# Kernel tuning notes

Measured on AMD Instinct MI355X. Metric: run time of the kernel, lower is better.

## Reference

```python
import jax, jax.numpy as jnp
import numpy as np

B, S, NX, NH = 2, 2048, 1024, 16
HD = NX // NH  # head dim = 64


def setup_inputs() -> dict:
    key = jax.random.key(0)
    k1, k2, k3 = jax.random.split(key, 3)
    x = jax.random.normal(k1, (B, S, NX), dtype=jnp.float32)
    w_attn = jax.random.normal(k2, (NX, 3 * NX), dtype=jnp.float32) * 0.02
    b_attn = jnp.zeros((3 * NX,), dtype=jnp.float32)
    w_proj = jax.random.normal(k3, (NX, NX), dtype=jnp.float32) * 0.02
    b_proj = jnp.zeros((NX,), dtype=jnp.float32)
    return {"x": x, "w_attn": w_attn, "b_attn": b_attn, "w_proj": w_proj, "b_proj": b_proj}


def _split_heads(t):
    # [B, S, NX] -> [B, NH, S, HD]
    b, s, _ = t.shape
    return t.reshape(b, s, NH, HD).transpose(0, 2, 1, 3)


def reference(x, w_attn, b_attn, w_proj, b_proj):
    # c_attn: Conv1D == affine projection to fused QKV
    qkv = jnp.einsum("bsi,io->bso", x, w_attn) + b_attn  # [B, S, 3*NX]
    q, k, v = jnp.split(qkv, 3, axis=2)
    q, k, v = _split_heads(q), _split_heads(k), _split_heads(v)  # [B, NH, S, HD]

    # scaled dot-product scores (scale=True)
    w = jnp.einsum("bhqd,bhkd->bhqk", q, k) / jnp.sqrt(jnp.asarray(HD, dtype=q.dtype))

    # causal mask via multiply-subtract (matches TF: w*b - 10000*(1-b))
    nd = ns = S
    i = jnp.arange(nd)[:, None]
    j = jnp.arange(ns)[None, :]
    b = (i >= j - ns + nd).astype(w.dtype)  # [nd, ns]
    w = w * b - 10000.0 * (1.0 - b)

    w = jax.nn.softmax(w, axis=-1)  # stable_softmax
    # attn_dropout / head_mask: identity (inference, no head mask)

    a = jnp.einsum("bhqk,bhkd->bhqd", w, v)  # [B, NH, S, HD]
    # merge heads -> [B, S, NX]
    a = a.transpose(0, 2, 1, 3).reshape(B, S, NX)
    # c_proj
    out = jnp.einsum("bsi,io->bso", a, w_proj) + b_proj
    return out
```

## Files before the change

### kernel.cpp

```cpp
#include <hip/hip_runtime.h>
#include <stdint.h>

typedef __attribute__((ext_vector_type(8))) short short8;
typedef __attribute__((ext_vector_type(4))) float f32x4;
typedef __attribute__((ext_vector_type(16))) float f32x16;
typedef __attribute__((ext_vector_type(4))) unsigned short ushort4v;
typedef __attribute__((ext_vector_type(2))) int int2v;

#define BB 2
#define SS 2048
#define NXDIM 1024
#define NHEADS 16
#define HDIM 64

__device__ __forceinline__ unsigned short f2bf(float f){
  unsigned int u = __float_as_uint(f);
  u += 0x7fffu + ((u >> 16) & 1u);
  return (unsigned short)(u >> 16);
}

__device__ __forceinline__ void gload_lds16(const void* g, void* l){
  __builtin_amdgcn_global_load_lds((const __attribute__((address_space(1))) void*)g,
                                   (__attribute__((address_space(3))) void*)l, 16, 0, 0);
}

__device__ __forceinline__ unsigned cvt_pk_bf16(float lo, float hi){
  unsigned r;
  asm("v_cvt_pk_bf16_f32 %0, %1, %2" : "=v"(r) : "v"(lo), "v"(hi));
  return r;
}

__device__ __forceinline__ int2v ds_tr_b16(unsigned addr){
  int2v r;
  asm volatile("ds_read_b64_tr_b16 %0, %1" : "=v"(r) : "v"(addr));
  return r;
}

__device__ __forceinline__ int2v plswap(int a, int b){
  return __builtin_amdgcn_permlane32_swap(a, b, false, false);
}
__device__ __forceinline__ float plmax(float x){
  int2v r = plswap(__float_as_int(x), __float_as_int(x));
  return fmaxf(__int_as_float(r.x), __int_as_float(r.y));
}
__device__ __forceinline__ float pladd(float x){
  int2v r = plswap(__float_as_int(x), __float_as_int(x));
  return __int_as_float(r.x) + __int_as_float(r.y);
}

__global__ __launch_bounds__(256) void prep_k(const float* __restrict__ x,
                                              unsigned short* __restrict__ xb,
                                              const float* __restrict__ wa,
                                              unsigned short* __restrict__ waT,
                                              const float* __restrict__ wp,
                                              unsigned short* __restrict__ wpT){
  __shared__ float t[32][33];
  int bid = blockIdx.x;
  if (bid < 4096){
    const int i = bid*256 + (int)threadIdx.x;
    float4 v = ((const float4*)x)[i];
    ushort4v r = { f2bf(v.x), f2bf(v.y), f2bf(v.z), f2bf(v.w) };
    ((ushort4v*)xb)[i] = r;
    return;
  }
  bid -= 4096;
  const int by = (bid >> 7) * 32;
  int bxi = bid & 127;
  const bool second = bxi >= 96;
  const float* in = second ? wp : wa;
  unsigned short* out = second ? wpT : waT;
  const int C = second ? 1024 : 3072;
  const int R = 1024;
  const int bx = (second ? (bxi - 96) : bxi) * 32;
  const int tx = threadIdx.x & 31, ty = threadIdx.x >> 5;
  #pragma unroll
  for (int i = ty; i < 32; i += 8)
    t[i][tx] = in[(size_t)(by + i) * C + bx + tx];
  __syncthreads();
  #pragma unroll
  for (int i = ty; i < 32; i += 8)
    out[(size_t)(bx + i) * R + by + tx] = f2bf(t[tx][i]);
}

__global__ __launch_bounds__(256) void gemm2_64_k(const unsigned short* __restrict__ A,
                                                  const unsigned short* __restrict__ BT,
                                                  const float* __restrict__ bias,
                                                  float* __restrict__ Cout,
                                                  int M, int N, int K)
{
  __shared__ unsigned short As[64*32];
  __shared__ unsigned short Bs[64*32];
  const int tid = threadIdx.x;
  const int w = tid >> 6, lane = tid & 63;
  const int l15 = lane & 15, g = lane >> 4;
  const int wr = w >> 1, wc = w & 1;
  const int m0 = blockIdx.y * 64, n0 = blockIdx.x * 64;

  f32x4 acc[2][2];
  #pragma unroll
  for (int m=0;m<2;m++)
    #pragma unroll
    for (int n=0;n<2;n++) acc[m][n] = (f32x4){0.f,0.f,0.f,0.f};

  const int srow_in = lane >> 2;
  const int scol = (lane & 3) * 8;

  for (int k0 = 0; k0 < K; k0 += 32){
    __syncthreads();
    gload_lds16(A  + (size_t)(m0 + w*16 + srow_in) * K + (k0 + scol), &As[(w*16)*32]);
    gload_lds16(BT + (size_t)(n0 + w*16 + srow_in) * K + (k0 + scol), &Bs[(w*16)*32]);
    __syncthreads();

    short8 af[2], bf[2];
    #pragma unroll
    for (int m=0;m<2;m++) af[m] = *(const short8*)&As[(wr*32 + m*16 + l15)*32 + g*8];
    #pragma unroll
    for (int n=0;n<2;n++) bf[n] = *(const short8*)&Bs[(wc*32 + n*16 + l15)*32 + g*8];
    #pragma unroll
    for (int m=0;m<2;m++)
      #pragma unroll
      for (int n=0;n<2;n++)
        acc[m][n] = __builtin_amdgcn_mfma_f32_16x16x32_bf16(af[m], bf[n], acc[m][n], 0, 0, 0);
  }

  const int crow0 = m0 + wr*32;
  const int ccol0 = n0 + wc*32;
  #pragma unroll
  for (int n=0;n<2;n++){
    const int col = ccol0 + n*16 + l15;
    const float bv = bias[col];
    #pragma unroll
    for (int m=0;m<2;m++){
      #pragma unroll
      for (int r=0;r<4;r++){
        const int row = crow0 + m*16 + g*4 + r;
        Cout[(size_t)row * N + col] = acc[m][n][r] + bv;
      }
    }
  }
}

__global__ __launch_bounds__(512) void gemm256_k(const unsigned short* __restrict__ A,
                                                 const unsigned short* __restrict__ BT,
                                                 const float* __restrict__ bias,
                                                 unsigned short* __restrict__ Cout,
                                                 int M, int N, int K)
{
  __shared__ unsigned short lds[57344];
  unsigned short* As0 = lds;
  unsigned short* Bs0 = lds + 32768;
  const int tid = threadIdx.x;
  const int w = tid >> 6, lane = tid & 63;
  const int l15 = lane & 15, g = lane >> 4;
  const int wm = w >> 2, wn = w & 3;
  const int m0 = blockIdx.y * 256, n0 = blockIdx.x * 192;

  f32x4 acc[8][3];
  #pragma unroll
  for (int m=0;m<8;m++)
    #pragma unroll
    for (int n=0;n<3;n++) acc[m][n] = (f32x4){0.f,0.f,0.f,0.f};

  const int srow = lane >> 3;
  const int scol = 8 * ((lane & 7) ^ (lane >> 3));

  auto stageA = [&](int bi, int k0, int j){
    const int r = w*32 + j*8 + srow;
    gload_lds16(A + (size_t)(m0 + r) * K + (k0 + scol), As0 + bi*16384 + (w*32 + j*8)*64);
  };
  auto stageB = [&](int bi, int k0, int j){
    const int r = w*24 + j*8 + srow;
    gload_lds16(BT + (size_t)(n0 + r) * K + (k0 + scol), Bs0 + bi*12288 + (w*24 + j*8)*64);
  };

  #pragma unroll
  for (int j=0;j<4;j++) stageA(0, 0, j);
  #pragma unroll
  for (int j=0;j<3;j++) stageB(0, 0, j);
  asm volatile("s_waitcnt vmcnt(0)" ::: "memory");
  __syncthreads();

  const int niter = K >> 6;
  int cur = 0;

  for (int t = 0; t < niter; ++t){
    const int k1 = (t+1) << 6;
    if (t+1 < niter){
      #pragma unroll
      for (int j=0;j<4;j++) stageA(cur^1, k1, j);
      #pragma unroll
      for (int j=0;j<3;j++) stageB(cur^1, k1, j);
    }

    const char* Ab = (const char*)(As0 + cur*16384);
    const char* Bb = (const char*)(Bs0 + cur*12288);

    short8 bf[3][2];
    #pragma unroll
    for (int nf=0;nf<3;nf++){
      const int row = wn*48 + nf*16 + l15;
      #pragma unroll
      for (int kk=0;kk<2;kk++)
        bf[nf][kk] = *(const short8*)(Bb + row*128 + ((kk*64 + g*16) ^ ((l15&7)<<4)));
    }

    #pragma unroll
    for (int ph=0; ph<4; ++ph){
      short8 af[2][2];
      #pragma unroll
      for (int i=0;i<2;i++){
        const int mf = ph*2 + i;
        const int row = wm*128 + mf*16 + l15;
        #pragma unroll
        for (int kk=0;kk<2;kk++)
          af[i][kk] = *(const short8*)(Ab + row*128 + ((kk*64 + g*16) ^ ((l15&7)<<4)));
      }
      asm volatile("s_waitcnt lgkmcnt(0)" ::: "memory");
      __builtin_amdgcn_sched_barrier(0);

      __builtin_amdgcn_s_setprio(1);
      #pragma unroll
      for (int i=0;i<2;i++)
        #pragma unroll
        for (int nf=0;nf<3;nf++)
          #pragma unroll
          for (int kk=0;kk<2;kk++)
            acc[ph*2+i][nf] = __builtin_amdgcn_mfma_f32_16x16x32_bf16(af[i][kk], bf[nf][kk],
                                                                      acc[ph*2+i][nf], 0, 0, 0);
      __builtin_amdgcn_s_setprio(0);
    }

    asm volatile("s_waitcnt vmcnt(0)" ::: "memory");
    __syncthreads();
    cur ^= 1;
  }

  unsigned short* ct = lds;
  #pragma unroll
  for (int nf=0;nf<3;nf++){
    const int col = wn*48 + nf*16 + l15;
    const float bv = bias[n0 + col];
    #pragma unroll
    for (int mf=0;mf<8;mf++){
      #pragma unroll
      for (int r=0;r<4;r++)
        ct[(wm*128 + mf*16 + g*4 + r)*192 + col] = f2bf(acc[mf][nf][r] + bv);
    }
  }
  __syncthreads();
  #pragma unroll
  for (int u = 0; u < 12; ++u){
    const int idx = u*512 + tid;
    const int row = idx / 24, sl = idx % 24;
    *(short8*)(Cout + (size_t)(m0 + row) * N + n0 + sl*8) = *(const short8*)&ct[row*192 + sl*8];
  }
}

__global__ __launch_bounds__(512) void attn_k(const unsigned short* __restrict__ qkv,
                                              unsigned short* __restrict__ aout)
{
  const int xy = ((int)blockIdx.x + (int)blockIdx.y) & 15;
  const int qb = blockIdx.z ? xy : (15 - xy);
  const int h = blockIdx.y, b = blockIdx.z;
  const int tid = threadIdx.x;
  const int w = tid >> 6, lane = tid & 63;
  const int l31 = lane & 31, hi = lane >> 5;
  const int qw = w >> 1, p = w & 1;

  __shared__ unsigned short lds[32768];
  unsigned short* Ksb = lds;
  unsigned short* Vsb = lds + 16384;

  const size_t rs = 3 * NXDIM;
  const unsigned short* Qg = qkv + (size_t)b * SS * rs + h * HDIM;
  const unsigned short* Kg = Qg + NXDIM;
  const unsigned short* Vg = Qg + 2 * NXDIM;

  const int q0w = qb*128 + qw*32;
  const int q   = q0w + l31;
  const int qw_hi = q0w + 31;

  short8 qf[4];
  #pragma unroll
  for (int c=0;c<4;c++)
    qf[c] = *(const short8*)(Qg + (size_t)q * rs + c*16 + 8*hi);

  f32x16 O0, O1;
  #pragma unroll
  for (int r=0;r<16;r++){ O0[r]=0.f; O1[r]=0.f; }
  float m_run = -1e30f, l_run = 0.f;
  const float SC2 = 0.125f * 1.44269504089f;
  const float THRR = 44.36f;

  const int krow_in = lane >> 3;
  const int kcol    = 8 * ((lane & 7) ^ (lane >> 3));
  const int v_d     = ((lane >> 3) & 3) * 16 + 8 * (lane & 1);
  const unsigned vtr_base = (unsigned)(size_t)Vsb + 8u*(unsigned)lane + 768u*(unsigned)hi;

  auto stage = [&](int bi, int tt){
    unsigned short* Kd = Ksb + (p*2 + bi)*4096;
    unsigned short* Vd = Vsb + (p*2 + bi)*4096;
    #pragma unroll
    for (int j=0;j<2;j++){
      const int ch = qw*2 + j;
      const int krow = tt*64 + ch*8 + krow_in;
      gload_lds16(Kg + (size_t)krow * rs + kcol, Kd + ch*512);
      const int vkv = tt*64 + (ch*2 + hi)*4 + ((lane>>1)&3);
      gload_lds16(Vg + (size_t)vkv * rs + v_d, Vd + ch*512);
    }
  };

  const int tmax = 2*qb + 1;
  stage(0, p);
  __syncthreads();
  int cur = 0;

  for (int t = p; t <= tmax; t += 2){
    if (t + 2 <= tmax) stage(cur^1, t+2);

    const char* Kb = (const char*)(Ksb + (p*2 + cur)*4096);
    const unsigned vb = vtr_base + (unsigned)((p*2 + cur)*8192);

    #pragma unroll
    for (int kvs=0;kvs<2;kvs++){
      const int kv_lo = t*64 + kvs*32;
      if (kv_lo > qw_hi) continue;

      f32x16 S;
      #pragma unroll
      for (int r=0;r<16;r++) S[r] = 0.f;
      __builtin_amdgcn_s_setprio(1);
      #pragma unroll
      for (int c=0;c<4;c++){
        const int row = kvs*32 + l31;
        short8 kf = *(const short8*)(Kb + row*128 + ((c*32 + 16*hi) ^ ((row&7)<<4)));
        S = __builtin_amdgcn_mfma_f32_32x32x16_bf16(kf, qf[c], S, 0, 0, 0);
      }
      __builtin_amdgcn_s_setprio(0);

      int2v tv[8];
      #pragma unroll
      for (int c=0;c<2;c++)
        #pragma unroll
        for (int dh=0;dh<2;dh++)
          #pragma unroll
          for (int eb=0;eb<2;eb++)
            tv[c*4+dh*2+eb] = ds_tr_b16(vb + (unsigned)((kvs*8 + c*4 + eb)*512 + dh*256));

      float mA=-1e30f, mB=-1e30f, mC=-1e30f, mD=-1e30f;
      if (kv_lo + 31 > q0w){
        #pragma unroll
        for (int r=0;r<16;r+=4){
          const int kvb = kv_lo + 8*(r>>2) + 4*hi;
          float s0 = (kvb+0 <= q) ? S[r+0] : -1e30f;
          float s1 = (kvb+1 <= q) ? S[r+1] : -1e30f;
          float s2 = (kvb+2 <= q) ? S[r+2] : -1e30f;
          float s3 = (kvb+3 <= q) ? S[r+3] : -1e30f;
          S[r+0]=s0; S[r+1]=s1; S[r+2]=s2; S[r+3]=s3;
          mA = fmaxf(mA, s0); mB = fmaxf(mB, s1); mC = fmaxf(mC, s2); mD = fmaxf(mD, s3);
        }
      } else {
        #pragma unroll
        for (int r=0;r<16;r+=4){
          mA = fmaxf(mA, S[r+0]); mB = fmaxf(mB, S[r+1]);
          mC = fmaxf(mC, S[r+2]); mD = fmaxf(mD, S[r+3]);
        }
      }
      float mx = fmaxf(fmaxf(mA,mB), fmaxf(mC,mD));
      mx = plmax(mx);

      if (!__all(mx <= m_run + THRR)){
        const float m_new = fmaxf(m_run, mx);
        const float corr = __builtin_exp2f((m_run - m_new) * SC2);
        m_run = m_new;
        l_run *= corr;
        #pragma unroll
        for (int r=0;r<16;r++){ O0[r] *= corr; O1[r] *= corr; }
      }
      const float msc = m_run * SC2;

      float lA=0.f, lB=0.f, lC=0.f, lD=0.f;
      #pragma unroll
      for (int r=0;r<16;r+=4){
        float p0=__builtin_exp2f(__builtin_fmaf(S[r+0],SC2,-msc));
        float p1=__builtin_exp2f(__builtin_fmaf(S[r+1],SC2,-msc));
        float p2=__builtin_exp2f(__builtin_fmaf(S[r+2],SC2,-msc));
        float p3=__builtin_exp2f(__builtin_fmaf(S[r+3],SC2,-msc));
        S[r+0]=p0; S[r+1]=p1; S[r+2]=p2; S[r+3]=p3;
        lA+=p0; lB+=p1; lC+=p2; lD+=p3;
      }
      float ls = (lA+lB) + (lC+lD);
      ls = pladd(ls);
      l_run += ls;

      unsigned pk[8];
      #pragma unroll
      for (int i=0;i<8;i++) pk[i] = cvt_pk_bf16(S[2*i], S[2*i+1]);
      short8 pfrag[2];
      #pragma unroll
      for (int c=0;c<2;c++){
        int2v r0 = plswap((int)pk[4*c+0], (int)pk[4*c+2]);
        int2v r1 = plswap((int)pk[4*c+1], (int)pk[4*c+3]);
        union { unsigned u[4]; short8 s; } pw;
        pw.u[0] = (unsigned)r0.x; pw.u[1] = (unsigned)r1.x;
        pw.u[2] = (unsigned)r0.y; pw.u[3] = (unsigned)r1.y;
        pfrag[c] = pw.s;
      }

      asm volatile("s_waitcnt lgkmcnt(0)" ::: "memory");
      __builtin_amdgcn_sched_barrier(0);

      __builtin_amdgcn_s_setprio(1);
      #pragma unroll
      for (int c=0;c<2;c++){
        union { int2v t[2]; short8 s; } v0, v1;
        v0.t[0] = tv[c*4+0]; v0.t[1] = tv[c*4+1];
        v1.t[0] = tv[c*4+2]; v1.t[1] = tv[c*4+3];
        O0 = __builtin_amdgcn_mfma_f32_32x32x16_bf16(v0.s, pfrag[c], O0, 0, 0, 0);
        O1 = __builtin_amdgcn_mfma_f32_32x32x16_bf16(v1.s, pfrag[c], O1, 0, 0, 0);
      }
      __builtin_amdgcn_s_setprio(0);
    }

    __syncthreads();
    cur ^= 1;
  }

  float* sm = (float*)lds + qw * (64*34);
  if (p){
    #pragma unroll
    for (int r=0;r<16;r++){ sm[lane*34 + r] = O0[r]; sm[lane*34 + 16 + r] = O1[r]; }
    sm[lane*34 + 32] = m_run;
    sm[lane*34 + 33] = l_run;
  }
  __syncthreads();
  if (!p){
    const float m1 = sm[lane*34 + 32], l1 = sm[lane*34 + 33];
    const float mm = fmaxf(m_run, m1);
    const float c0 = __builtin_exp2f((m_run - mm) * SC2);
    const float c1 = __builtin_exp2f((m1 - mm) * SC2);
    const float inv = 1.f / (l_run*c0 + l1*c1);
    unsigned short* dst = aout + ((size_t)b*SS + q) * NXDIM + h*HDIM;
    #pragma unroll
    for (int g4=0; g4<4; g4++){
      ushort4v a0, a1;
      #pragma unroll
      for (int i=0;i<4;i++){
        a0[i] = f2bf((O0[4*g4+i]*c0 + sm[lane*34 + 4*g4+i]*c1) * inv);
        a1[i] = f2bf((O1[4*g4+i]*c0 + sm[lane*34 + 16 + 4*g4+i]*c1) * inv);
      }
      *(ushort4v*)(dst + 8*g4 + 4*hi)      = a0;
      *(ushort4v*)(dst + 32 + 8*g4 + 4*hi) = a1;
    }
  }
}

extern "C" void kernel_launch(void* const* d_in, const int* in_sizes, int n_in,
                              void* d_out, int out_size, void* d_ws, size_t ws_size,
                              hipStream_t stream){
  (void)in_sizes; (void)n_in; (void)out_size; (void)ws_size;
  const float* x      = (const float*)d_in[0];
  const float* w_attn = (const float*)d_in[1];
  const float* b_attn = (const float*)d_in[2];
  const float* w_proj = (const float*)d_in[3];
  const float* b_proj = (const float*)d_in[4];
  float* out = (float*)d_out;

  unsigned short* xb   = (unsigned short*)d_ws;
  unsigned short* waT  = xb  + (size_t)4096*1024;
  unsigned short* wpT  = waT + (size_t)3072*1024;
  unsigned short* qkv  = wpT + (size_t)1024*1024;
  unsigned short* aout = qkv + (size_t)4096*3072;

  prep_k<<<8192, 256, 0, stream>>>(x, xb, w_attn, waT, w_proj, wpT);
  gemm256_k<<<dim3(3072/192, 4096/256), 512, 0, stream>>>(xb, waT, b_attn, qkv, 4096, 3072, 1024);
  attn_k<<<dim3(SS/128, NHEADS, BB), 512, 0, stream>>>(qkv, aout);
  gemm2_64_k<<<dim3(1024/64, 4096/64), 256, 0, stream>>>(aout, wpT, b_proj, out, 4096, 1024, 1024);
}
```

Measured before the change: 108.0 us.

## Shrink QKV GEMM tile to 128x192 with 32-wide K steps

Replaces the 256x192 block tile of the QKV projection GEMM with a 128x192 tile and a K step of 32 instead of 64, using a new XOR swizzle and a smaller LDS footprint. The grid doubles from 256 to 512 blocks, so the 256 CUs get more even coverage and LDS use per block drops, which may let more blocks reside per CU. In exchange each block reuses loaded data less, runs more K iterations with a barrier per step, and has fewer MFMAs between syncs to hide load latency.

```diff
diff --git a/kernel.cpp b/kernel.cpp
--- a/kernel.cpp
+++ b/kernel.cpp
@@ -140,116 +140,91 @@
   }
 }
 
-__global__ __launch_bounds__(512) void gemm256_k(const unsigned short* __restrict__ A,
+__global__ __launch_bounds__(512) void gemm128_k(const unsigned short* __restrict__ A,
                                                  const unsigned short* __restrict__ BT,
                                                  const float* __restrict__ bias,
                                                  unsigned short* __restrict__ Cout,
                                                  int M, int N, int K)
 {
-  __shared__ unsigned short lds[57344];
-  unsigned short* As0 = lds;
-  unsigned short* Bs0 = lds + 32768;
+  __shared__ unsigned short lds[24576];
   const int tid = threadIdx.x;
   const int w = tid >> 6, lane = tid & 63;
   const int l15 = lane & 15, g = lane >> 4;
   const int wm = w >> 2, wn = w & 3;
-  const int m0 = blockIdx.y * 256, n0 = blockIdx.x * 192;
-
-  f32x4 acc[8][3];
-  #pragma unroll
-  for (int m=0;m<8;m++)
+  const int m0 = blockIdx.y * 128, n0 = blockIdx.x * 192;
+
+  f32x4 acc[4][3];
+  #pragma unroll
+  for (int m=0;m<4;m++)
     #pragma unroll
     for (int n=0;n<3;n++) acc[m][n] = (f32x4){0.f,0.f,0.f,0.f};
 
-  const int srow = lane >> 3;
-  const int scol = 8 * ((lane & 7) ^ (lane >> 3));
-
-  auto stageA = [&](int bi, int k0, int j){
-    const int r = w*32 + j*8 + srow;
-    gload_lds16(A + (size_t)(m0 + r) * K + (k0 + scol), As0 + bi*16384 + (w*32 + j*8)*64);
+  const int srow_in = lane >> 2;
+  const int sscol   = 8 * ((lane & 3) ^ ((lane >> 2) & 3));
+
+  auto stage = [&](int bi, int kt){
+    const int k0 = kt * 32;
+    unsigned short* Ad = lds + bi*4096;
+    unsigned short* Bd = lds + 8192 + bi*6144;
+    gload_lds16(A + (size_t)(m0 + w*16 + srow_in) * K + (k0 + sscol), Ad + (w*16)*32);
+    gload_lds16(BT + (size_t)(n0 + w*16 + srow_in) * K + (k0 + sscol), Bd + (w*16)*32);
+    if (w < 4)
+      gload_lds16(BT + (size_t)(n0 + (8+w)*16 + srow_in) * K + (k0 + sscol), Bd + ((8+w)*16)*32);
   };
-  auto stageB = [&](int bi, int k0, int j){
-    const int r = w*24 + j*8 + srow;
-    gload_lds16(BT + (size_t)(n0 + r) * K + (k0 + scol), Bs0 + bi*12288 + (w*24 + j*8)*64);
-  };
-
-  #pragma unroll
-  for (int j=0;j<4;j++) stageA(0, 0, j);
-  #pragma unroll
-  for (int j=0;j<3;j++) stageB(0, 0, j);
+
+  const int nt = K >> 5;
+  stage(0, 0);
   asm volatile("s_waitcnt vmcnt(0)" ::: "memory");
   __syncthreads();
 
-  const int niter = K >> 6;
-  int cur = 0;
-
-  for (int t = 0; t < niter; ++t){
-    const int k1 = (t+1) << 6;
-    if (t+1 < niter){
-      #pragma unroll
-      for (int j=0;j<4;j++) stageA(cur^1, k1, j);
-      #pragma unroll
-      for (int j=0;j<3;j++) stageB(cur^1, k1, j);
-    }
-
-    const char* Ab = (const char*)(As0 + cur*16384);
-    const char* Bb = (const char*)(Bs0 + cur*12288);
-
-    short8 bf[3][2];
-    #pragma unroll
-    for (int nf=0;nf<3;nf++){
-      const int row = wn*48 + nf*16 + l15;
-      #pragma unroll
-      for (int kk=0;kk<2;kk++)
-        bf[nf][kk] = *(const short8*)(Bb + row*128 + ((kk*64 + g*16) ^ ((l15&7)<<4)));
-    }
-
-    #pragma unroll
-    for (int ph=0; ph<4; ++ph){
-      short8 af[2][2];
-      #pragma unroll
-      for (int i=0;i<2;i++){
-        const int mf = ph*2 + i;
-        const int row = wm*128 + mf*16 + l15;
-        #pragma unroll
-        for (int kk=0;kk<2;kk++)
-          af[i][kk] = *(const short8*)(Ab + row*128 + ((kk*64 + g*16) ^ ((l15&7)<<4)));
-      }
-      asm volatile("s_waitcnt lgkmcnt(0)" ::: "memory");
-      __builtin_amdgcn_sched_barrier(0);
-
-      __builtin_amdgcn_s_setprio(1);
-      #pragma unroll
-      for (int i=0;i<2;i++)
-        #pragma unroll
-        for (int nf=0;nf<3;nf++)
-          #pragma unroll
-          for (int kk=0;kk<2;kk++)
-            acc[ph*2+i][nf] = __builtin_amdgcn_mfma_f32_16x16x32_bf16(af[i][kk], bf[nf][kk],
-                                                                      acc[ph*2+i][nf], 0, 0, 0);
-      __builtin_amdgcn_s_setprio(0);
-    }
+  for (int t = 0; t < nt; ++t){
+    const int bi = t & 1;
+    if (t + 1 < nt) stage(bi^1, t+1);
+
+    const char* Ab = (const char*)(lds + bi*4096);
+    const char* Bb = (const char*)(lds + 8192 + bi*6144);
+
+    short8 af[4], bf[3];
+    #pragma unroll
+    for (int m=0;m<4;m++){
+      const int row = wm*64 + m*16 + l15;
+      af[m] = *(const short8*)(Ab + row*64 + 16*(g ^ (row&3)));
+    }
+    #pragma unroll
+    for (int n=0;n<3;n++){
+      const int row = wn*48 + n*16 + l15;
+      bf[n] = *(const short8*)(Bb + row*64 + 16*(g ^ (row&3)));
+    }
+    asm volatile("s_waitcnt lgkmcnt(0)" ::: "memory");
+    __builtin_amdgcn_sched_barrier(0);
+
+    __builtin_amdgcn_s_setprio(1);
+    #pragma unroll
+    for (int m=0;m<4;m++)
+      #pragma unroll
+      for (int n=0;n<3;n++)
+        acc[m][n] = __builtin_amdgcn_mfma_f32_16x16x32_bf16(af[m], bf[n], acc[m][n], 0, 0, 0);
+    __builtin_amdgcn_s_setprio(0);
 
     asm volatile("s_waitcnt vmcnt(0)" ::: "memory");
     __syncthreads();
-    cur ^= 1;
   }
 
   unsigned short* ct = lds;
   #pragma unroll
-  for (int nf=0;nf<3;nf++){
-    const int col = wn*48 + nf*16 + l15;
+  for (int n=0;n<3;n++){
+    const int col = wn*48 + n*16 + l15;
     const float bv = bias[n0 + col];
     #pragma unroll
-    for (int mf=0;mf<8;mf++){
+    for (int m=0;m<4;m++){
       #pragma unroll
       for (int r=0;r<4;r++)
-        ct[(wm*128 + mf*16 + g*4 + r)*192 + col] = f2bf(acc[mf][nf][r] + bv);
+        ct[(wm*64 + m*16 + g*4 + r)*192 + col] = f2bf(acc[m][n][r] + bv);
     }
   }
   __syncthreads();
   #pragma unroll
-  for (int u = 0; u < 12; ++u){
+  for (int u = 0; u < 6; ++u){
     const int idx = u*512 + tid;
     const int row = idx / 24, sl = idx % 24;
     *(short8*)(Cout + (size_t)(m0 + row) * N + n0 + sl*8) = *(const short8*)&ct[row*192 + sl*8];
@@ -473,7 +448,7 @@
   unsigned short* aout = qkv + (size_t)4096*3072;
 
   prep_k<<<8192, 256, 0, stream>>>(x, xb, w_attn, waT, w_proj, wpT);
-  gemm256_k<<<dim3(3072/192, 4096/256), 512, 0, stream>>>(xb, waT, b_attn, qkv, 4096, 3072, 1024);
+  gemm128_k<<<dim3(3072/192, 4096/128), 512, 0, stream>>>(xb, waT, b_attn, qkv, 4096, 3072, 1024);
   attn_k<<<dim3(SS/128, NHEADS, BB), 512, 0, stream>>>(qkv, aout);
   gemm2_64_k<<<dim3(1024/64, 4096/64), 256, 0, stream>>>(aout, wpT, b_proj, out, 4096, 1024, 1024);
 }
```

New measurement: 112.1 us. 1.04x slower.
